# Kernel optimization log

Measured on AMD Instinct MI355X. Metric: run time of the kernel, lower is better.

## Reference

```python
import jax, jax.numpy as jnp
import numpy as np

EPS = 1e-5
BLEND = 0.5  # with prior_batchsize=0, x_iclm == x_bn so CNM == BatchNorm1d (training mode)


def batchnorm(x, gamma, beta):
    # torch BatchNorm1d training mode: batch mean, biased variance
    mean = x.mean(axis=0)
    var = x.var(axis=0)  # ddof=0 (biased), matching torch normalization
    xn = (x - mean) * jax.lax.rsqrt(var + EPS)
    return xn * gamma + beta


def ensemble_linear(x, W):
    # x: [B, D*F], W: [D, O, F] block-diagonal weights
    B = x.shape[0]
    D, O, F = W.shape
    xb = x.reshape(B, D, F)
    out = jnp.einsum('bdf,dof->bdo', xb, W)
    return out.reshape(B, D * O)


def setup_inputs() -> dict:
    key = jax.random.key(0)
    ks = jax.random.split(key, 3)
    B, F, D, O2 = 16384, 1024, 4, 32
    x = jax.random.normal(ks[0], (B, F), dtype=jnp.float32)
    # torch init: normal_(mean=0, std=0.0001) on linear weights
    W1 = jax.random.normal(ks[1], (D, F, F), dtype=jnp.float32) * 1e-4
    W2 = jax.random.normal(ks[2], (D, O2, F), dtype=jnp.float32) * 1e-4
    g1 = jnp.ones((D * F,), jnp.float32); b1 = jnp.zeros((D * F,), jnp.float32)
    g2 = jnp.ones((D * F,), jnp.float32); b2 = jnp.zeros((D * F,), jnp.float32)
    g3 = jnp.ones((D * O2,), jnp.float32); b3 = jnp.zeros((D * O2,), jnp.float32)
    return {"x": x, "W1": W1, "W2": W2, "g1": g1, "b1": b1,
            "g2": g2, "b2": b2, "g3": g3, "b3": b3}


def reference(x, W1, W2, g1, b1, g2, b2, g3, b3):
    D = W1.shape[0]
    h = jnp.concatenate([x] * D, axis=-1)          # [B, D*F]
    h = batchnorm(h, g1, b1)                        # CNM 1
    h = ensemble_linear(h, W1)                      # EnsembleLinear F->F
    h = jax.nn.sigmoid(batchnorm(h, g2, b2))        # CNM 2 + Sigmoid
    h = ensemble_linear(h, W2)                      # EnsembleLinear F->32
    h = jax.nn.sigmoid(batchnorm(h, g3, b3))        # CNM 3 + Sigmoid
    return h  # [B, D*32]
```

## Files before the change

kernel.cpp:

```cpp
#include <hip/hip_runtime.h>
#include <hip/hip_bf16.h>
#include <stdint.h>

#define B_N 16384
#define F_N 1024
#define D_N 4
#define O_N 32
#define NCOL1 (D_N * F_N)
#define NCOL2 (D_N * O_N)

static constexpr float EPS = 1e-5f;

typedef __bf16 bf16x8 __attribute__((ext_vector_type(8)));
typedef __bf16 bf16x4 __attribute__((ext_vector_type(4)));
typedef float  f32x4  __attribute__((ext_vector_type(4)));

#define GLD16(gp, lp)                                                          \
  __builtin_amdgcn_global_load_lds(                                            \
      (__attribute__((address_space(1))) void*)(uintptr_t)(gp),                \
      (__attribute__((address_space(3))) void*)(lp), 16, 0, 0)

__global__ __launch_bounds__(256) void k_stats_x_conv(
    const float* __restrict__ x, float* __restrict__ part,
    __bf16* __restrict__ xb) {
  int t = threadIdx.x, blk = blockIdx.x;
  const float4* xr = (const float4*)x;
  float s0 = 0, s1 = 0, s2 = 0, s3 = 0, q0 = 0, q1 = 0, q2 = 0, q3 = 0;
  int r0 = blk * 64;
  for (int r = r0; r < r0 + 64; ++r) {
    float4 v = xr[(size_t)r * (F_N / 4) + t];
    s0 += v.x; q0 += v.x * v.x;
    s1 += v.y; q1 += v.y * v.y;
    s2 += v.z; q2 += v.z * v.z;
    s3 += v.w; q3 += v.w * v.w;
    bf16x4 o;
    o[0] = (__bf16)v.x; o[1] = (__bf16)v.y; o[2] = (__bf16)v.z; o[3] = (__bf16)v.w;
    *(bf16x4*)(xb + (size_t)r * F_N + t * 4) = o;
  }
  float* p = part + (size_t)blk * 2048;
  p[t * 4 + 0] = s0; p[t * 4 + 1] = s1; p[t * 4 + 2] = s2; p[t * 4 + 3] = s3;
  p[1024 + t * 4 + 0] = q0; p[1024 + t * 4 + 1] = q1;
  p[1024 + t * 4 + 2] = q2; p[1024 + t * 4 + 3] = q3;
}

__global__ __launch_bounds__(256) void k_stats_x_final(
    const float* __restrict__ part, float* __restrict__ rstdx) {
  int c = blockIdx.x * 256 + threadIdx.x;
  float s = 0, q = 0;
  for (int b = 0; b < 256; ++b) {
    s += part[(size_t)b * 2048 + c];
    q += part[(size_t)b * 2048 + 1024 + c];
  }
  float mean = s * (1.0f / B_N);
  float var = q * (1.0f / B_N) - mean * mean;
  rstdx[c] = rsqrtf(var + EPS);
}

__global__ __launch_bounds__(256) void k_fold_w1(const float* __restrict__ W1,
                                                 const float* __restrict__ g1,
                                                 const float* __restrict__ rstdx,
                                                 __bf16* __restrict__ W1b) {
  size_t base = (size_t)(blockIdx.x * 256 + threadIdx.x) * 4;
  int f = (int)(base & (F_N - 1));
  int d = (int)(base >> 20);
  float4 w = *(const float4*)(W1 + base);
  float4 g = *(const float4*)(g1 + d * F_N + f);
  float4 r = *(const float4*)(rstdx + f);
  bf16x4 o;
  o[0] = (__bf16)(w.x * g.x * r.x); o[1] = (__bf16)(w.y * g.y * r.y);
  o[2] = (__bf16)(w.z * g.z * r.z); o[3] = (__bf16)(w.w * g.w * r.w);
  *(bf16x4*)(W1b + base) = o;
}

__global__ __launch_bounds__(256) void k_fold_w2(const float* __restrict__ W2,
                                                 __bf16* __restrict__ W2b) {
  size_t base = (size_t)(blockIdx.x * 256 + threadIdx.x) * 4;
  float4 w = *(const float4*)(W2 + base);
  bf16x4 o;
  o[0] = (__bf16)w.x; o[1] = (__bf16)w.y; o[2] = (__bf16)w.z; o[3] = (__bf16)w.w;
  *(bf16x4*)(W2b + base) = o;
}

__global__ __launch_bounds__(512, 2) void k_gemm1(
    const __bf16* __restrict__ A, const __bf16* __restrict__ Bw,
    __bf16* __restrict__ C, float* __restrict__ p2s, float* __restrict__ p2q) {
  __shared__ __bf16 ldsA[2][2][256 * 32];
  __shared__ __bf16 ldsB[2][2][256 * 32];
  const int tid = threadIdx.x;
  const int wave = tid >> 6, lane = tid & 63;
  const int wm = wave >> 2, wn = wave & 3;
  int bid = (int)blockIdx.x;
  const int c_ = bid & 7, q_ = bid >> 3;
  const int bm = c_ * 8 + (q_ >> 4), bn = q_ & 15;
  const int m0 = bm * 256, n0 = bn * 256;
  const int fr = lane & 15, kg = lane >> 4;
  const int swz8 = (kg ^ ((fr >> 1) & 3)) * 8;
  const int srow = tid >> 2;
  const int scb = ((tid & 3) ^ ((tid >> 3) & 3)) * 16;
  const char* Ab = (const char*)A + (size_t)(m0 + srow) * (F_N * 2) + scb;
  const char* Bb = (const char*)Bw + (size_t)(n0 + srow) * (F_N * 2) + scb;
  char* ldsAx = (char*)&ldsA[0][0][0];
  char* ldsBx = (char*)&ldsB[0][0][0];
  const int wo = wave * 1024;

#define SA(buf_, kk_, kb_)                                                     \
  do {                                                                         \
    GLD16(Ab + (kb_) + (kk_) * 64,                                             \
          ldsAx + (buf_) * 32768 + (kk_) * 16384 + wo);                        \
    GLD16(Ab + 128 * (F_N * 2) + (kb_) + (kk_) * 64,                           \
          ldsAx + (buf_) * 32768 + (kk_) * 16384 + 8192 + wo);                 \
  } while (0)
#define SBv(buf_, kk_, kb_)                                                    \
  do {                                                                         \
    GLD16(Bb + (kb_) + (kk_) * 64,                                             \
          ldsBx + (buf_) * 32768 + (kk_) * 16384 + wo);                        \
    GLD16(Bb + 128 * (F_N * 2) + (kb_) + (kk_) * 64,                           \
          ldsBx + (buf_) * 32768 + (kk_) * 16384 + 8192 + wo);                 \
  } while (0)
#define LDA4(dst_, buf_, kk_, qm_)                                             \
  { _Pragma("unroll") for (int i_ = 0; i_ < 4; ++i_)                           \
      dst_[i_] = *(const bf16x8*)&ldsA[buf_][kk_]                              \
          [(wm * 128 + (qm_) * 64 + i_ * 16 + fr) * 32 + swz8]; }
#define LDB4(dst_, buf_, kk_)                                                  \
  { _Pragma("unroll") for (int i_ = 0; i_ < 4; ++i_)                           \
      dst_[i_] = *(const bf16x8*)&ldsB[buf_][kk_]                              \
          [(wn * 64 + i_ * 16 + fr) * 32 + swz8]; }
#define MFMA16(a_, b_, qm_)                                                    \
  { _Pragma("unroll") for (int i_ = 0; i_ < 4; ++i_)                           \
      _Pragma("unroll") for (int j_ = 0; j_ < 4; ++j_)                         \
        acc[(qm_) * 4 + i_][j_] = __builtin_amdgcn_mfma_f32_16x16x32_bf16(     \
            a_[i_], b_[j_], acc[(qm_) * 4 + i_][j_], 0, 0, 0); }
#define BAR() __builtin_amdgcn_s_barrier()
#define SB0() __builtin_amdgcn_sched_barrier(0)
#define WAITVM4() asm volatile("s_waitcnt vmcnt(4)" ::: "memory")
#define PRIO1() __builtin_amdgcn_s_setprio(1)
#define PRIO0() __builtin_amdgcn_s_setprio(0)

  f32x4 acc[8][4] = {};
  bf16x8 afrE[4], afrO[4], bfrE[4], bfrO[4];

  SBv(0, 0, 0); SA(0, 0, 0); SBv(0, 1, 0); SA(0, 1, 0);
  asm volatile("s_waitcnt vmcnt(4)" ::: "memory");
  BAR(); SB0();
  LDA4(afrE, 0, 0, 0); LDB4(bfrE, 0, 0);

#define TILE(b_, nb_, kn_)                                                     \
  SBv(nb_, 0, kn_); BAR(); SB0();                                              \
  LDA4(afrO, b_, 0, 1);                                                        \
  PRIO1(); MFMA16(afrE, bfrE, 0); PRIO0();                                     \
  SA(nb_, 0, kn_); WAITVM4(); BAR(); SB0();                                    \
  LDA4(afrE, b_, 1, 0); LDB4(bfrO, b_, 1);                                     \
  PRIO1(); MFMA16(afrO, bfrE, 1); PRIO0();                                     \
  SBv(nb_, 1, kn_); BAR(); SB0();                                              \
  LDA4(afrO, b_, 1, 1);                                                        \
  PRIO1(); MFMA16(afrE, bfrO, 0); PRIO0();                                     \
  SA(nb_, 1, kn_); WAITVM4(); BAR(); SB0();                                    \
  LDA4(afrE, nb_, 0, 0); LDB4(bfrE, nb_, 0);                                   \
  PRIO1(); MFMA16(afrO, bfrO, 1); PRIO0();

  for (int t = 0; t < 16; t += 2) {
    const int kn1 = (t + 1) * 128;
    const int kn2 = (t + 2 < 16) ? (t + 2) * 128 : 0;
    TILE(0, 1, kn1)
    TILE(1, 0, kn2)
  }

  const int cr = kg * 4, cc = fr;
#pragma unroll
  for (int mi = 0; mi < 8; ++mi)
#pragma unroll
    for (int ni = 0; ni < 4; ++ni) {
      int row = m0 + wm * 128 + mi * 16 + cr;
      int col = n0 + wn * 64 + ni * 16 + cc;
#pragma unroll
      for (int r = 0; r < 4; ++r)
        C[(size_t)(row + r) * NCOL1 + col] = (__bf16)acc[mi][ni][r];
    }

  float* srs = (float*)&ldsA[1][0][0];
  float* srq = srs + 512;
  __syncthreads();
#pragma unroll
  for (int ni = 0; ni < 4; ++ni) {
    float ss = 0, qq = 0;
#pragma unroll
    for (int mi = 0; mi < 8; ++mi) {
      f32x4 v = acc[mi][ni];
#pragma unroll
      for (int r = 0; r < 4; ++r) { ss += v[r]; qq += v[r] * v[r]; }
    }
    ss += __shfl_xor(ss, 16); ss += __shfl_xor(ss, 32);
    qq += __shfl_xor(qq, 16); qq += __shfl_xor(qq, 32);
    if (lane < 16) {
      srs[wave * 64 + ni * 16 + lane] = ss;
      srq[wave * 64 + ni * 16 + lane] = qq;
    }
  }
  __syncthreads();
  if (tid < 256) {
    int j = tid, wnn = j >> 6, jj = j & 63;
    float S = srs[wnn * 64 + jj] + srs[(4 + wnn) * 64 + jj];
    float Q = srq[wnn * 64 + jj] + srq[(4 + wnn) * 64 + jj];
    p2s[(size_t)bm * NCOL1 + n0 + j] = S;
    p2q[(size_t)bm * NCOL1 + n0 + j] = Q;
  }
#undef SA
#undef SBv
#undef LDA4
#undef LDB4
#undef MFMA16
#undef TILE
#undef BAR
#undef SB0
#undef WAITVM4
#undef PRIO1
#undef PRIO0
}

__global__ __launch_bounds__(256) void k_stats2_final(
    const float* __restrict__ p2s, const float* __restrict__ p2q,
    const float* __restrict__ g2, const float* __restrict__ b2,
    float* __restrict__ a2, float* __restrict__ c2) {
  int c = blockIdx.x * 256 + threadIdx.x;
  float s = 0, q = 0;
  for (int b = 0; b < 64; ++b) {
    s += p2s[(size_t)b * NCOL1 + c];
    q += p2q[(size_t)b * NCOL1 + c];
  }
  float mean = s * (1.0f / B_N);
  float var = q * (1.0f / B_N) - mean * mean;
  float rstd = rsqrtf(var + EPS);
  float aa = rstd * g2[c];
  a2[c] = aa;
  c2[c] = b2[c] - mean * aa;
}

__global__ __launch_bounds__(256) void k_gemm2(
    const __bf16* __restrict__ G1, const __bf16* __restrict__ W2b,
    const float* __restrict__ a2, const float* __restrict__ c2,
    float* __restrict__ out2, float* __restrict__ p3s,
    float* __restrict__ p3q) {
  __shared__ float sred[2][4][2][16];
  const int tid = threadIdx.x;
  const int wave = tid >> 6, lane = tid & 63;
  const int m0 = blockIdx.x * 64;
  const int d = blockIdx.y;
  const int fr = lane & 15, fk = (lane >> 4) * 8;
  const __bf16* Arow = G1 + (size_t)(m0 + wave * 16 + fr) * NCOL1 + d * F_N;
  const __bf16* Wd = W2b + (size_t)d * O_N * F_N;
  const float* ap = a2 + d * F_N;
  const float* cp = c2 + d * F_N;
  f32x4 acc[2] = {};
#pragma unroll 2
  for (int k0 = 0; k0 < F_N; k0 += 32) {
    bf16x8 av = *(const bf16x8*)(Arow + k0 + fk);
    f32x4 aa0 = *(const f32x4*)(ap + k0 + fk);
    f32x4 aa1 = *(const f32x4*)(ap + k0 + fk + 4);
    f32x4 cc0 = *(const f32x4*)(cp + k0 + fk);
    f32x4 cc1 = *(const f32x4*)(cp + k0 + fk + 4);
    bf16x8 af;
#pragma unroll
    for (int j = 0; j < 4; ++j) {
      float v = (float)av[j] * aa0[j] + cc0[j];
      af[j] = (__bf16)(1.0f / (1.0f + __expf(-v)));
    }
#pragma unroll
    for (int j = 0; j < 4; ++j) {
      float v = (float)av[4 + j] * aa1[j] + cc1[j];
      af[4 + j] = (__bf16)(1.0f / (1.0f + __expf(-v)));
    }
    bf16x8 b0 = *(const bf16x8*)(Wd + (size_t)fr * F_N + k0 + fk);
    bf16x8 b1 = *(const bf16x8*)(Wd + (size_t)(16 + fr) * F_N + k0 + fk);
    acc[0] = __builtin_amdgcn_mfma_f32_16x16x32_bf16(af, b0, acc[0], 0, 0, 0);
    acc[1] = __builtin_amdgcn_mfma_f32_16x16x32_bf16(af, b1, acc[1], 0, 0, 0);
  }
  const int cr = (lane >> 4) * 4, cc = lane & 15;
#pragma unroll
  for (int n = 0; n < 2; ++n)
#pragma unroll
    for (int r = 0; r < 4; ++r)
      out2[(size_t)(m0 + wave * 16 + cr + r) * NCOL2 + d * O_N + n * 16 + cc] =
          acc[n][r];

#pragma unroll
  for (int n = 0; n < 2; ++n) {
    float s = acc[n][0] + acc[n][1] + acc[n][2] + acc[n][3];
    float q = acc[n][0] * acc[n][0] + acc[n][1] * acc[n][1] +
              acc[n][2] * acc[n][2] + acc[n][3] * acc[n][3];
    s += __shfl_xor(s, 16); s += __shfl_xor(s, 32);
    q += __shfl_xor(q, 16); q += __shfl_xor(q, 32);
    if (lane < 16) {
      sred[0][wave][n][lane] = s;
      sred[1][wave][n][lane] = q;
    }
  }
  __syncthreads();
  if (tid < 32) {
    int n = tid >> 4, c = tid & 15;
    float S = sred[0][0][n][c] + sred[0][1][n][c] + sred[0][2][n][c] +
              sred[0][3][n][c];
    float Q = sred[1][0][n][c] + sred[1][1][n][c] + sred[1][2][n][c] +
              sred[1][3][n][c];
    int col = d * O_N + n * 16 + c;
    p3s[(size_t)blockIdx.x * NCOL2 + col] = S;
    p3q[(size_t)blockIdx.x * NCOL2 + col] = Q;
  }
}

__global__ __launch_bounds__(128) void k_stats3_final(
    const float* __restrict__ p3s, const float* __restrict__ p3q,
    const float* __restrict__ g3, const float* __restrict__ b3,
    float* __restrict__ a3, float* __restrict__ c3) {
  int c = threadIdx.x;
  float s = 0, q = 0;
  for (int b = 0; b < 256; ++b) {
    s += p3s[(size_t)b * NCOL2 + c];
    q += p3q[(size_t)b * NCOL2 + c];
  }
  float mean = s * (1.0f / B_N);
  float var = q * (1.0f / B_N) - mean * mean;
  float rstd = rsqrtf(var + EPS);
  float aa = rstd * g3[c];
  a3[c] = aa;
  c3[c] = b3[c] - mean * aa;
}

__global__ __launch_bounds__(256) void k_final(const float* __restrict__ out2,
                                               const float* __restrict__ a3,
                                               const float* __restrict__ c3,
                                               float* __restrict__ out) {
  size_t base = (size_t)(blockIdx.x * 256 + threadIdx.x) * 4;
  int c = (int)(base & (NCOL2 - 1));
  f32x4 v = *(const f32x4*)(out2 + base);
  f32x4 a = *(const f32x4*)(a3 + c);
  f32x4 cc = *(const f32x4*)(c3 + c);
  f32x4 o;
#pragma unroll
  for (int j = 0; j < 4; ++j)
    o[j] = 1.0f / (1.0f + __expf(-(v[j] * a[j] + cc[j])));
  *(f32x4*)(out + base) = o;
}

extern "C" void kernel_launch(void* const* d_in, const int* in_sizes, int n_in,
                              void* d_out, int out_size, void* d_ws,
                              size_t ws_size, hipStream_t stream) {
  (void)in_sizes; (void)n_in; (void)out_size; (void)ws_size;
  const float* x = (const float*)d_in[0];
  const float* W1 = (const float*)d_in[1];
  const float* W2 = (const float*)d_in[2];
  const float* g1 = (const float*)d_in[3];
  const float* g2 = (const float*)d_in[5];
  const float* b2 = (const float*)d_in[6];
  const float* g3 = (const float*)d_in[7];
  const float* b3 = (const float*)d_in[8];
  float* out = (float*)d_out;

  char* ws = (char*)d_ws;
  size_t off = 0;
  auto alloc = [&](size_t bytes) -> void* {
    void* p = ws + off;
    off = (off + bytes + 255) & ~(size_t)255;
    return p;
  };
  float* rstdx = (float*)alloc((size_t)F_N * 4);
  float* a2 = (float*)alloc((size_t)NCOL1 * 4);
  float* c2 = (float*)alloc((size_t)NCOL1 * 4);
  float* a3 = (float*)alloc((size_t)NCOL2 * 4);
  float* c3 = (float*)alloc((size_t)NCOL2 * 4);
  float* part1 = (float*)alloc((size_t)256 * 2048 * 4);
  float* p2s = (float*)alloc((size_t)64 * NCOL1 * 4);
  float* p2q = (float*)alloc((size_t)64 * NCOL1 * 4);
  float* p3s = (float*)alloc((size_t)256 * NCOL2 * 4);
  float* p3q = (float*)alloc((size_t)256 * NCOL2 * 4);
  __bf16* W1b = (__bf16*)alloc((size_t)D_N * F_N * F_N * 2);
  __bf16* W2b = (__bf16*)alloc((size_t)D_N * O_N * F_N * 2);
  __bf16* xb = (__bf16*)alloc((size_t)B_N * F_N * 2);
  __bf16* G1 = (__bf16*)alloc((size_t)B_N * NCOL1 * 2);
  float* out2 = (float*)alloc((size_t)B_N * NCOL2 * 4);

  k_stats_x_conv<<<256, 256, 0, stream>>>(x, part1, xb);
  k_stats_x_final<<<4, 256, 0, stream>>>(part1, rstdx);
  k_fold_w1<<<4096, 256, 0, stream>>>(W1, g1, rstdx, W1b);
  k_fold_w2<<<128, 256, 0, stream>>>(W2, W2b);
  k_gemm1<<<1024, 512, 0, stream>>>(xb, W1b, G1, p2s, p2q);
  k_stats2_final<<<16, 256, 0, stream>>>(p2s, p2q, g2, b2, a2, c2);
  k_gemm2<<<dim3(256, 4), 256, 0, stream>>>(G1, W2b, a2, c2, out2, p3s, p3q);
  k_stats3_final<<<1, 128, 0, stream>>>(p3s, p3q, g3, b3, a3, c3);
  k_final<<<2048, 256, 0, stream>>>(out2, a3, c3, out);
}
```

Before: 267.5 us.

## Restructure GEMM1 main loop into a four-slot LDS ring with three-deep prefetch

```diff
diff --git a/kernel.cpp b/kernel.cpp
--- a/kernel.cpp
+++ b/kernel.cpp
@@ -84,8 +84,8 @@
 __global__ __launch_bounds__(512, 2) void k_gemm1(
     const __bf16* __restrict__ A, const __bf16* __restrict__ Bw,
     __bf16* __restrict__ C, float* __restrict__ p2s, float* __restrict__ p2q) {
-  __shared__ __bf16 ldsA[2][2][256 * 32];
-  __shared__ __bf16 ldsB[2][2][256 * 32];
+  __shared__ __bf16 ldsA[4][256 * 32];
+  __shared__ __bf16 ldsB[4][256 * 32];
   const int tid = threadIdx.x;
   const int wave = tid >> 6, lane = tid & 63;
   const int wm = wave >> 2, wn = wave & 3;
@@ -99,31 +99,27 @@
   const int scb = ((tid & 3) ^ ((tid >> 3) & 3)) * 16;
   const char* Ab = (const char*)A + (size_t)(m0 + srow) * (F_N * 2) + scb;
   const char* Bb = (const char*)Bw + (size_t)(n0 + srow) * (F_N * 2) + scb;
-  char* ldsAx = (char*)&ldsA[0][0][0];
-  char* ldsBx = (char*)&ldsB[0][0][0];
+  char* ldsAx = (char*)&ldsA[0][0];
+  char* ldsBx = (char*)&ldsB[0][0];
   const int wo = wave * 1024;
 
-#define SA(buf_, kk_, kb_)                                                     \
+#define SA(slot_, kb_)                                                         \
   do {                                                                         \
-    GLD16(Ab + (kb_) + (kk_) * 64,                                             \
-          ldsAx + (buf_) * 32768 + (kk_) * 16384 + wo);                        \
-    GLD16(Ab + 128 * (F_N * 2) + (kb_) + (kk_) * 64,                           \
-          ldsAx + (buf_) * 32768 + (kk_) * 16384 + 8192 + wo);                 \
+    GLD16(Ab + (kb_), ldsAx + (slot_) * 16384 + wo);                           \
+    GLD16(Ab + 128 * (F_N * 2) + (kb_), ldsAx + (slot_) * 16384 + 8192 + wo);  \
   } while (0)
-#define SBv(buf_, kk_, kb_)                                                    \
+#define SBv(slot_, kb_)                                                        \
   do {                                                                         \
-    GLD16(Bb + (kb_) + (kk_) * 64,                                             \
-          ldsBx + (buf_) * 32768 + (kk_) * 16384 + wo);                        \
-    GLD16(Bb + 128 * (F_N * 2) + (kb_) + (kk_) * 64,                           \
-          ldsBx + (buf_) * 32768 + (kk_) * 16384 + 8192 + wo);                 \
+    GLD16(Bb + (kb_), ldsBx + (slot_) * 16384 + wo);                           \
+    GLD16(Bb + 128 * (F_N * 2) + (kb_), ldsBx + (slot_) * 16384 + 8192 + wo);  \
   } while (0)
-#define LDA4(dst_, buf_, kk_, qm_)                                             \
+#define LDA4(dst_, slot_, qm_)                                                 \
   { _Pragma("unroll") for (int i_ = 0; i_ < 4; ++i_)                           \
-      dst_[i_] = *(const bf16x8*)&ldsA[buf_][kk_]                              \
+      dst_[i_] = *(const bf16x8*)&ldsA[slot_]                                  \
           [(wm * 128 + (qm_) * 64 + i_ * 16 + fr) * 32 + swz8]; }
-#define LDB4(dst_, buf_, kk_)                                                  \
+#define LDB4(dst_, slot_)                                                      \
   { _Pragma("unroll") for (int i_ = 0; i_ < 4; ++i_)                           \
-      dst_[i_] = *(const bf16x8*)&ldsB[buf_][kk_]                              \
+      dst_[i_] = *(const bf16x8*)&ldsB[slot_]                                  \
           [(wn * 64 + i_ * 16 + fr) * 32 + swz8]; }
 #define MFMA16(a_, b_, qm_)                                                    \
   { _Pragma("unroll") for (int i_ = 0; i_ < 4; ++i_)                           \
@@ -132,38 +128,35 @@
             a_[i_], b_[j_], acc[(qm_) * 4 + i_][j_], 0, 0, 0); }
 #define BAR() __builtin_amdgcn_s_barrier()
 #define SB0() __builtin_amdgcn_sched_barrier(0)
-#define WAITVM4() asm volatile("s_waitcnt vmcnt(4)" ::: "memory")
 #define PRIO1() __builtin_amdgcn_s_setprio(1)
 #define PRIO0() __builtin_amdgcn_s_setprio(0)
 
   f32x4 acc[8][4] = {};
-  bf16x8 afrE[4], afrO[4], bfrE[4], bfrO[4];
-
-  SBv(0, 0, 0); SA(0, 0, 0); SBv(0, 1, 0); SA(0, 1, 0);
-  asm volatile("s_waitcnt vmcnt(4)" ::: "memory");
-  BAR(); SB0();
-  LDA4(afrE, 0, 0, 0); LDB4(bfrE, 0, 0);
-
-#define TILE(b_, nb_, kn_)                                                     \
-  SBv(nb_, 0, kn_); BAR(); SB0();                                              \
-  LDA4(afrO, b_, 0, 1);                                                        \
-  PRIO1(); MFMA16(afrE, bfrE, 0); PRIO0();                                     \
-  SA(nb_, 0, kn_); WAITVM4(); BAR(); SB0();                                    \
-  LDA4(afrE, b_, 1, 0); LDB4(bfrO, b_, 1);                                     \
-  PRIO1(); MFMA16(afrO, bfrE, 1); PRIO0();                                     \
-  SBv(nb_, 1, kn_); BAR(); SB0();                                              \
-  LDA4(afrO, b_, 1, 1);                                                        \
-  PRIO1(); MFMA16(afrE, bfrO, 0); PRIO0();                                     \
-  SA(nb_, 1, kn_); WAITVM4(); BAR(); SB0();                                    \
-  LDA4(afrE, nb_, 0, 0); LDB4(bfrE, nb_, 0);                                   \
-  PRIO1(); MFMA16(afrO, bfrO, 1); PRIO0();
-
-  for (int t = 0; t < 16; t += 2) {
-    const int kn1 = (t + 1) * 128;
-    const int kn2 = (t + 2 < 16) ? (t + 2) * 128 : 0;
-    TILE(0, 1, kn1)
-    TILE(1, 0, kn2)
-  }
+  bf16x8 afr0[4], afr1[4], bfr[4];
+
+  SBv(0, 0);   SA(0, 0);
+  SBv(1, 64);  SA(1, 64);
+  SBv(2, 128); SA(2, 128);
+
+#define REGION(rb_, sb_, kb_, SOK_, VN_)                                       \
+  asm volatile("s_waitcnt vmcnt(" #VN_ ")" ::: "memory");                      \
+  BAR(); SB0();                                                                \
+  if (SOK_) { SBv(sb_, kb_); SA(sb_, kb_); }                                   \
+  LDB4(bfr, rb_); LDA4(afr0, rb_, 0); LDA4(afr1, rb_, 1);                      \
+  PRIO1(); MFMA16(afr0, bfr, 0); MFMA16(afr1, bfr, 1); PRIO0();
+
+  for (int T = 0; T < 28; T += 4) {
+    const int kb0 = (T + 3) * 64, kb1 = (T + 4) * 64;
+    const int kb2 = (T + 5) * 64, kb3 = (T + 6) * 64;
+    REGION(0, 3, kb0, 1, 8)
+    REGION(1, 0, kb1, 1, 8)
+    REGION(2, 1, kb2, 1, 8)
+    REGION(3, 2, kb3, 1, 8)
+  }
+  REGION(0, 3, 1984, 1, 8)
+  REGION(1, 0, 0, 0, 8)
+  REGION(2, 0, 0, 0, 4)
+  REGION(3, 0, 0, 0, 0)
 
   const int cr = kg * 4, cc = fr;
 #pragma unroll
@@ -177,7 +170,7 @@
         C[(size_t)(row + r) * NCOL1 + col] = (__bf16)acc[mi][ni][r];
     }
 
-  float* srs = (float*)&ldsA[1][0][0];
+  float* srs = (float*)&ldsA[0][0];
   float* srq = srs + 512;
   __syncthreads();
 #pragma unroll
@@ -209,10 +202,9 @@
 #undef LDA4
 #undef LDB4
 #undef MFMA16
-#undef TILE
+#undef REGION
 #undef BAR
 #undef SB0
-#undef WAITVM4
 #undef PRIO1
 #undef PRIO0
 }
```

Result: slower. 277.8 us (+3.8%).
